# Optimization experiments

Measured on AMD Instinct MI355X. Metric: run time of the kernel, lower is better.

## Reference

```python
import jax, jax.numpy as jnp
import numpy as np


def setup_inputs() -> dict:
    key = jax.random.key(0)
    ks = jax.random.split(key, 6)
    B, S, D = 2, 2048, 1024
    E, DFF = 8, 2048  # E includes always-on expert 0; router sees E-1 routed experts
    scale = 0.02
    return {
        "hidden_states": jax.random.normal(ks[0], (B, S, D), dtype=jnp.float32),
        "router_w": jax.random.normal(ks[1], (D, E - 1), dtype=jnp.float32) * scale,
        "router_b": jnp.zeros((E - 1,), dtype=jnp.float32),
        "wg": jax.random.normal(ks[2], (E, D, DFF), dtype=jnp.float32) * scale,
        "wu": jax.random.normal(ks[3], (E, D, DFF), dtype=jnp.float32) * scale,
        "wd": jax.random.normal(ks[4], (E, DFF, D), dtype=jnp.float32) * scale,
        "top_k": 2,
    }


def _expert_mlp(x, wg_e, wu_e, wd_e):
    # SwiGLU MLP: down( silu(x @ gate) * (x @ up) )
    return (jax.nn.silu(x @ wg_e) * (x @ wu_e)) @ wd_e


def reference(hidden_states, router_w, router_b, wg, wu, wd, top_k):
    B, S, D = hidden_states.shape
    E = wg.shape[0]  # total experts incl. always-on expert 0
    x = hidden_states.reshape(-1, D)  # [T, D]
    T = x.shape[0]

    # Router over E-1 routed experts, softmax in float32
    router_logits = x @ router_w + router_b  # [T, E-1]
    probs = jax.nn.softmax(router_logits.astype(jnp.float32), axis=-1)
    topw, topi = jax.lax.top_k(probs, top_k)  # [T, k]
    topw = topw / jnp.sum(topw, axis=-1, keepdims=True)
    topw = topw.astype(x.dtype)

    # Dense combine weights over routed experts (0 for unselected)
    cw = jnp.zeros((T, E - 1), dtype=x.dtype)
    cw = cw.at[jnp.arange(T)[:, None], topi].add(topw)  # [T, E-1]

    # Always-on expert 0 with weight 1
    out = _expert_mlp(x, wg[0], wu[0], wd[0])  # [T, D]

    # Routed experts 1..E-1 (static small loop over experts)
    for e in range(1, E):
        ye = _expert_mlp(x, wg[e], wu[e], wd[e])  # [T, D]
        out = out + cw[:, e - 1, None] * ye

    return out.reshape(B, S, -1)
```

## Files before the change

kernel.cpp:

```cpp
#include <hip/hip_runtime.h>

#define T_TOK 4096
#define DIM   1024
#define DFF   2048
#define NE    8
#define NR    7
#define MAXNB 71
#define NY    (32 + MAXNB)

typedef __bf16 bf16x8 __attribute__((ext_vector_type(8)));
typedef float  floatx4 __attribute__((ext_vector_type(4)));

__device__ __forceinline__ unsigned short f32_bf16(float f) {
  union { float f; unsigned int u; } v; v.f = f;
  unsigned int u = v.u;
  unsigned int r = (u + 0x7FFFu + ((u >> 16) & 1u)) >> 16;
  return (unsigned short)r;
}

typedef __attribute__((address_space(3))) void lds_void_t;
typedef const __attribute__((address_space(1))) void g_void_t;

__device__ __forceinline__ void gld16(const void* g, void* l) {
  __builtin_amdgcn_global_load_lds((g_void_t*)g, (lds_void_t*)l, 16, 0, 0);
}

__global__ __launch_bounds__(256) void cvt_x_kernel(const float4* __restrict__ in,
                                                    ushort4* __restrict__ out) {
  int i = blockIdx.x * 256 + threadIdx.x;
  float4 v = in[i];
  ushort4 o;
  o.x = f32_bf16(v.x); o.y = f32_bf16(v.y);
  o.z = f32_bf16(v.z); o.w = f32_bf16(v.w);
  out[i] = o;
}

__global__ __launch_bounds__(256) void router_kernel(const float* __restrict__ x,
                                                     const float* __restrict__ rw,
                                                     const float* __restrict__ rb,
                                                     int* __restrict__ idxR,
                                                     float* __restrict__ wslR,
                                                     int* __restrict__ cnt,
                                                     int4* __restrict__ tokE,
                                                     float2* __restrict__ tokW) {
  const int lane = threadIdx.x & 63;
  const int t = blockIdx.x * 4 + (threadIdx.x >> 6);
  const float* xr = x + (size_t)t * DIM;
  float acc[NR];
#pragma unroll
  for (int e = 0; e < NR; e++) acc[e] = 0.f;
  for (int d = lane; d < DIM; d += 64) {
    float xv = xr[d];
#pragma unroll
    for (int e = 0; e < NR; e++) acc[e] += xv * rw[d * NR + e];
  }
#pragma unroll
  for (int off = 32; off > 0; off >>= 1) {
#pragma unroll
    for (int e = 0; e < NR; e++) acc[e] += __shfl_xor(acc[e], off, 64);
  }
  if (lane == 0) {
    float lg[NR];
    float m = -1e30f;
#pragma unroll
    for (int e = 0; e < NR; e++) { lg[e] = acc[e] + rb[e]; m = fmaxf(m, lg[e]); }
    float p[NR], s = 0.f;
#pragma unroll
    for (int e = 0; e < NR; e++) { p[e] = expf(lg[e] - m); s += p[e]; }
#pragma unroll
    for (int e = 0; e < NR; e++) p[e] /= s;
    int i1 = 0;
#pragma unroll
    for (int e = 1; e < NR; e++) if (p[e] > p[i1]) i1 = e;
    int i2 = (i1 == 0) ? 1 : 0;
#pragma unroll
    for (int e = 0; e < NR; e++) if (e != i1 && p[e] > p[i2]) i2 = e;
    float w1 = p[i1], w2 = p[i2], sw = w1 + w2;
    float w1n = w1 / sw, w2n = w2 / sw;
    int s1 = atomicAdd(&cnt[i1], 1);
    idxR[i1 * 4096 + s1] = t; wslR[i1 * 4096 + s1] = w1n;
    int s2 = atomicAdd(&cnt[i2], 1);
    idxR[i2 * 4096 + s2] = t; wslR[i2 * 4096 + s2] = w2n;
    int4 te; te.x = i1; te.y = s1; te.z = i2; te.w = s2;
    tokE[t] = te;
    float2 tw; tw.x = w1n; tw.y = w2n;
    tokW[t] = tw;
  }
}

__global__ __launch_bounds__(256) void sched_kernel(const int* __restrict__ cnt,
                                                    int* __restrict__ idxR,
                                                    float* __restrict__ wslR,
                                                    int4* __restrict__ schedAll,
                                                    int4* __restrict__ schedP,
                                                    int* __restrict__ prefOut,
                                                    int rsb) {
  __shared__ int nb[NR], pref[NR];
  if (threadIdx.x == 0) {
    int p = 0;
    for (int e = 0; e < NR; e++) { int c = cnt[e]; int n = (c + 127) >> 7; nb[e] = n; pref[e] = p; p += n; }
  }
  __syncthreads();
  if (threadIdx.x < NR) prefOut[threadIdx.x] = pref[threadIdx.x];
  for (int e = 0; e < NR; e++) {
    int c = cnt[e], top = nb[e] * 128;
    for (int i = c + (int)threadIdx.x; i < top; i += 256) {
      idxR[e * 4096 + i] = 0; wslR[e * 4096 + i] = 0.f;
    }
  }
  const int NBtot = pref[NR - 1] + nb[NR - 1];
  for (int y = threadIdx.x; y < 32; y += 256) {
    int4 ent; ent.x = 0; ent.y = -1; ent.z = y * 128; ent.w = 0;
    schedAll[y] = ent;
  }
  for (int y = threadIdx.x; y < MAXNB; y += 256) {
    int4 ent; ent.x = -1; ent.y = 0; ent.z = 0; ent.w = 0;
    if (y < NBtot) {
#pragma unroll
      for (int e = 0; e < NR; e++)
        if (y >= pref[e] && y < pref[e] + nb[e]) {
          int rb2 = y - pref[e];
          ent.x = e + 1; ent.y = e * 4096 + rb2 * 128; ent.z = rsb + y * 128;
        }
    }
    schedAll[32 + y] = ent;
  }
  for (int i = threadIdx.x; i < NR * 32; i += 256) {
    int e = i >> 5, rb2 = i & 31;
    int4 ent; ent.w = 0;
    if (rb2 < nb[e]) { ent.x = e + 1; ent.y = e * 4096 + rb2 * 128; ent.z = rb2 * 128; }
    else             { ent.x = -1; ent.y = 0; ent.z = 0; }
    schedP[i] = ent;
  }
}

__global__ __launch_bounds__(256) void transpose_cvt_kernel(
    const float* __restrict__ wg, const float* __restrict__ wu, const float* __restrict__ wd,
    unsigned short* __restrict__ wgt, unsigned short* __restrict__ wut,
    unsigned short* __restrict__ wdt) {
  __shared__ float tile[64][33];
  const int z = blockIdx.z;
  const float* src; unsigned short* dst; int R, C;
  if (z < 8)       { src = wg + (size_t)z * DIM * DFF;        dst = wgt + (size_t)z * DIM * DFF;        R = DIM; C = DFF; }
  else if (z < 16) { src = wu + (size_t)(z - 8) * DIM * DFF;  dst = wut + (size_t)(z - 8) * DIM * DFF;  R = DIM; C = DFF; }
  else             { src = wd + (size_t)(z - 16) * DFF * DIM; dst = wdt + (size_t)(z - 16) * DFF * DIM; R = DFF; C = DIM; }
  const int c0 = blockIdx.x * 32, r0 = blockIdx.y * 64;
  if (c0 >= C || r0 >= R) return;
  const int tx = threadIdx.x & 31, ty = threadIdx.x >> 5;
#pragma unroll
  for (int j = ty; j < 64; j += 8)
    tile[j][tx] = src[(size_t)(r0 + j) * C + c0 + tx];
  __syncthreads();
#pragma unroll
  for (int j = ty; j < 32; j += 8) {
    unsigned int lo = f32_bf16(tile[2 * tx][j]);
    unsigned int hi = f32_bf16(tile[2 * tx + 1][j]);
    *(unsigned int*)(dst + (size_t)(c0 + j) * R + r0 + 2 * tx) = lo | (hi << 16);
  }
}

__global__ __launch_bounds__(512, 2) void gemm1_kernel(
    const unsigned short* __restrict__ xb, const unsigned short* __restrict__ wgt,
    const unsigned short* __restrict__ wut, const int* __restrict__ idxR,
    const int4* __restrict__ sched, unsigned short* __restrict__ h, int gy) {
  const int nblk = gridDim.x;
  int bid = blockIdx.x;
  { int q = nblk >> 3, r = nblk & 7, xc = bid & 7, p = bid >> 3;
    bid = (xc < r ? xc * (q + 1) : r * (q + 1) + (xc - r) * q) + p; }
  const int bx = bid / gy, by = bid - bx * gy;
  const int4 ent = sched[by];
  if (ent.x < 0) return;
  __shared__ unsigned short smem[3 * 24576];
  const int tid = threadIdx.x, lane = tid & 63, wid = tid >> 6;
  const int n0 = bx * 128;
  const int wm64 = (wid >> 2) * 64, wn32 = (wid & 3) * 32;
  const int fr = lane & 15, kq8 = lane >> 4, x7 = fr & 7;
  const int r0 = tid >> 3;
  const int c8 = ((tid & 7) ^ (r0 & 7)) * 8;
  int tok0, tok1;
  if (ent.y < 0) { tok0 = ent.z + r0; tok1 = ent.z + r0 + 64; }
  else           { tok0 = idxR[ent.y + r0]; tok1 = idxR[ent.y + r0 + 64]; }
  const unsigned short* wgt_e = wgt + (size_t)ent.x * DIM * DFF;
  const unsigned short* wut_e = wut + (size_t)ent.x * DIM * DFF;
  const unsigned short* gA0 = xb + (size_t)tok0 * DIM + c8;
  const unsigned short* gA1 = xb + (size_t)tok1 * DIM + c8;
  const unsigned short* gG0 = wgt_e + (size_t)(n0 + r0) * DIM + c8;
  const unsigned short* gG1 = gG0 + (size_t)64 * DIM;
  const unsigned short* gU0 = wut_e + (size_t)(n0 + r0) * DIM + c8;
  const unsigned short* gU1 = gU0 + (size_t)64 * DIM;
  int offA[4][2], offB[2][2];
#pragma unroll
  for (int mi = 0; mi < 4; mi++)
#pragma unroll
    for (int kk = 0; kk < 2; kk++)
      offA[mi][kk] = (wm64 + mi * 16 + fr) * 64 + (((kk * 4 + kq8) ^ x7) * 8);
#pragma unroll
  for (int ni = 0; ni < 2; ni++)
#pragma unroll
    for (int kk = 0; kk < 2; kk++)
      offB[ni][kk] = (wn32 + ni * 16 + fr) * 64 + (((kk * 4 + kq8) ^ x7) * 8);
  floatx4 accg[4][2], accu[4][2];
  const floatx4 z4 = {0.f, 0.f, 0.f, 0.f};
#pragma unroll
  for (int i = 0; i < 4; i++)
#pragma unroll
    for (int j = 0; j < 2; j++) { accg[i][j] = z4; accu[i][j] = z4; }
  {
    unsigned short* d = smem + tid * 8;
    gld16(gA0, d);             gld16(gA1, d + 4096);
    gld16(gG0, d + 8192);      gld16(gG1, d + 12288);
    gld16(gU0, d + 16384);     gld16(gU1, d + 20480);
    unsigned short* e = smem + 24576 + tid * 8;
    gld16(gA0 + 64, e);        gld16(gA1 + 64, e + 4096);
    gld16(gG0 + 64, e + 8192); gld16(gG1 + 64, e + 12288);
    gld16(gU0 + 64, e + 16384); gld16(gU1 + 64, e + 20480);
  }
  asm volatile("s_waitcnt vmcnt(6)" ::: "memory");
  __builtin_amdgcn_s_barrier();
  int b = 0;
  for (int k = 0; k < 16; ++k) {
    const unsigned short* Bb = smem + b * 24576;
    int b2 = b + 2; if (b2 >= 3) b2 -= 3;
    unsigned short* db2 = smem + b2 * 24576 + tid * 8;
    if (k < 14) {
      const int kt = (k + 2) * 64;
      gld16(gA0 + kt, db2);         gld16(gA1 + kt, db2 + 4096);
      gld16(gG0 + kt, db2 + 8192);  gld16(gG1 + kt, db2 + 12288);
      gld16(gU0 + kt, db2 + 16384); gld16(gU1 + kt, db2 + 20480);
    }
    __builtin_amdgcn_sched_barrier(0);
    bf16x8 a[4][2], bg[2][2], bu[2][2];
#pragma unroll
    for (int mi = 0; mi < 4; mi++)
#pragma unroll
      for (int kk = 0; kk < 2; kk++) a[mi][kk] = *(const bf16x8*)(Bb + offA[mi][kk]);
#pragma unroll
    for (int ni = 0; ni < 2; ni++)
#pragma unroll
      for (int kk = 0; kk < 2; kk++) {
        bg[ni][kk] = *(const bf16x8*)(Bb + 8192 + offB[ni][kk]);
        bu[ni][kk] = *(const bf16x8*)(Bb + 16384 + offB[ni][kk]);
      }
    __builtin_amdgcn_s_setprio(1);
#pragma unroll
    for (int mi = 0; mi < 4; mi++)
#pragma unroll
      for (int ni = 0; ni < 2; ni++)
#pragma unroll
        for (int kk = 0; kk < 2; kk++)
          accg[mi][ni] = __builtin_amdgcn_mfma_f32_16x16x32_bf16(a[mi][kk], bg[ni][kk], accg[mi][ni], 0, 0, 0);
#pragma unroll
    for (int mi = 0; mi < 4; mi++)
#pragma unroll
      for (int ni = 0; ni < 2; ni++)
#pragma unroll
        for (int kk = 0; kk < 2; kk++)
          accu[mi][ni] = __builtin_amdgcn_mfma_f32_16x16x32_bf16(a[mi][kk], bu[ni][kk], accu[mi][ni], 0, 0, 0);
    __builtin_amdgcn_s_setprio(0);
    __builtin_amdgcn_sched_barrier(0);
    if (k < 14)       asm volatile("s_waitcnt vmcnt(6)" ::: "memory");
    else if (k == 14) asm volatile("s_waitcnt vmcnt(0)" ::: "memory");
    __builtin_amdgcn_s_barrier();
    b++; if (b == 3) b = 0;
  }
  const int rb = kq8 * 4;
#pragma unroll
  for (int mi = 0; mi < 4; mi++)
#pragma unroll
    for (int ni = 0; ni < 2; ni++)
#pragma unroll
      for (int r = 0; r < 4; r++) {
        int row = ent.z + wm64 + mi * 16 + rb + r;
        int col = n0 + wn32 + ni * 16 + fr;
        float g = accg[mi][ni][r], u = accu[mi][ni][r];
        float hv = (g / (1.f + __expf(-g))) * u;
        h[(size_t)row * DFF + col] = f32_bf16(hv);
      }
}

__global__ __launch_bounds__(512, 2) void gemm2_kernel(
    const unsigned short* __restrict__ hsrc, const unsigned short* __restrict__ wdt,
    const int4* __restrict__ sched, float* __restrict__ y, int gx) {
  const int nblk = gridDim.x;
  int bid = blockIdx.x;
  { int q = nblk >> 3, r = nblk & 7, xc = bid & 7, p = bid >> 3;
    bid = (xc < r ? xc * (q + 1) : r * (q + 1) + (xc - r) * q) + p; }
  const int by = bid / gx, bx = bid - by * gx;
  const int4 ent = sched[by];
  if (ent.x < 0) return;
  __shared__ unsigned short smem[3 * 24576];
  const int tid = threadIdx.x, lane = tid & 63, wid = tid >> 6;
  const int n0 = bx * 256;
  const int wm64 = (wid >> 2) * 64, wn64 = (wid & 3) * 64;
  const int fr = lane & 15, kq8 = lane >> 4, x7 = fr & 7;
  const int r0 = tid >> 3;
  const int c8 = ((tid & 7) ^ (r0 & 7)) * 8;
  const unsigned short* wdt_e = wdt + (size_t)ent.x * DFF * DIM;
  const unsigned short* gA0 = hsrc + (size_t)(ent.z + r0) * DFF + c8;
  const unsigned short* gA1 = gA0 + (size_t)64 * DFF;
  const unsigned short* gB0 = wdt_e + (size_t)(n0 + r0) * DFF + c8;
  const unsigned short* gB1 = gB0 + (size_t)64 * DFF;
  const unsigned short* gB2 = gB0 + (size_t)128 * DFF;
  const unsigned short* gB3 = gB0 + (size_t)192 * DFF;
  int offA[4][2], offB[2][2];
#pragma unroll
  for (int mi = 0; mi < 4; mi++)
#pragma unroll
    for (int kk = 0; kk < 2; kk++)
      offA[mi][kk] = (wm64 + mi * 16 + fr) * 64 + (((kk * 4 + kq8) ^ x7) * 8);
#pragma unroll
  for (int ni = 0; ni < 2; ni++)
#pragma unroll
    for (int kk = 0; kk < 2; kk++)
      offB[ni][kk] = (wn64 + ni * 16 + fr) * 64 + (((kk * 4 + kq8) ^ x7) * 8);
  floatx4 acc[4][4];
  const floatx4 z4 = {0.f, 0.f, 0.f, 0.f};
#pragma unroll
  for (int i = 0; i < 4; i++)
#pragma unroll
    for (int j = 0; j < 4; j++) acc[i][j] = z4;
  {
    unsigned short* d = smem + tid * 8;
    gld16(gA0, d);             gld16(gA1, d + 4096);
    gld16(gB0, d + 8192);      gld16(gB1, d + 12288);
    gld16(gB2, d + 16384);     gld16(gB3, d + 20480);
    unsigned short* e = smem + 24576 + tid * 8;
    gld16(gA0 + 64, e);        gld16(gA1 + 64, e + 4096);
    gld16(gB0 + 64, e + 8192); gld16(gB1 + 64, e + 12288);
    gld16(gB2 + 64, e + 16384); gld16(gB3 + 64, e + 20480);
  }
  asm volatile("s_waitcnt vmcnt(6)" ::: "memory");
  __builtin_amdgcn_s_barrier();
  int b = 0;
  for (int k = 0; k < 32; ++k) {
    const unsigned short* Bb = smem + b * 24576;
    int b2 = b + 2; if (b2 >= 3) b2 -= 3;
    unsigned short* db2 = smem + b2 * 24576 + tid * 8;
    if (k < 30) {
      const int kt = (k + 2) * 64;
      gld16(gA0 + kt, db2);         gld16(gA1 + kt, db2 + 4096);
      gld16(gB0 + kt, db2 + 8192);  gld16(gB1 + kt, db2 + 12288);
      gld16(gB2 + kt, db2 + 16384); gld16(gB3 + kt, db2 + 20480);
    }
    __builtin_amdgcn_sched_barrier(0);
    bf16x8 a[4][2], b0[2][2], b1[2][2];
#pragma unroll
    for (int mi = 0; mi < 4; mi++)
#pragma unroll
      for (int kk = 0; kk < 2; kk++) a[mi][kk] = *(const bf16x8*)(Bb + offA[mi][kk]);
#pragma unroll
    for (int ni = 0; ni < 2; ni++)
#pragma unroll
      for (int kk = 0; kk < 2; kk++) {
        b0[ni][kk] = *(const bf16x8*)(Bb + 8192 + offB[ni][kk]);
        b1[ni][kk] = *(const bf16x8*)(Bb + 10240 + offB[ni][kk]);
      }
    __builtin_amdgcn_s_setprio(1);
#pragma unroll
    for (int mi = 0; mi < 4; mi++)
#pragma unroll
      for (int ni = 0; ni < 2; ni++)
#pragma unroll
        for (int kk = 0; kk < 2; kk++) {
          acc[mi][ni]     = __builtin_amdgcn_mfma_f32_16x16x32_bf16(a[mi][kk], b0[ni][kk], acc[mi][ni], 0, 0, 0);
          acc[mi][2 + ni] = __builtin_amdgcn_mfma_f32_16x16x32_bf16(a[mi][kk], b1[ni][kk], acc[mi][2 + ni], 0, 0, 0);
        }
    __builtin_amdgcn_s_setprio(0);
    __builtin_amdgcn_sched_barrier(0);
    if (k < 30)       asm volatile("s_waitcnt vmcnt(6)" ::: "memory");
    else if (k == 30) asm volatile("s_waitcnt vmcnt(0)" ::: "memory");
    __builtin_amdgcn_s_barrier();
    b++; if (b == 3) b = 0;
  }
  const int rb = kq8 * 4;
#pragma unroll
  for (int mi = 0; mi < 4; mi++)
#pragma unroll
    for (int ni = 0; ni < 4; ni++)
#pragma unroll
      for (int r = 0; r < 4; r++)
        y[(size_t)(ent.z + wm64 + mi * 16 + rb + r) * DIM + n0 + wn64 + ni * 16 + fr] = acc[mi][ni][r];
}

__global__ __launch_bounds__(256) void gemm2_atomic_kernel(
    const unsigned short* __restrict__ h, const unsigned short* __restrict__ wdt,
    const int* __restrict__ idxR, const float* __restrict__ wslR,
    const int4* __restrict__ sched, float* __restrict__ out) {
  const int4 ent = sched[blockIdx.y];
  if (ent.x < 0) return;
  __shared__ unsigned short As[128 * 32];
  __shared__ unsigned short Bs[128 * 32];
  const int tid = threadIdx.x, lane = tid & 63, wid = tid >> 6;
  const int n0 = blockIdx.x * 128;
  const int wm = (wid >> 1) * 64, wn = (wid & 1) * 64;
  floatx4 acc[4][4];
  const floatx4 z4 = {0.f, 0.f, 0.f, 0.f};
#pragma unroll
  for (int i = 0; i < 4; i++)
#pragma unroll
    for (int j = 0; j < 4; j++) acc[i][j] = z4;
  const unsigned short* wdt_e = wdt + (size_t)ent.x * DFF * DIM;
  const int srow = tid >> 2, scol = (tid & 3) * 8;
  const unsigned short* ap0 = h + (size_t)(ent.z + srow) * DFF + scol;
  const unsigned short* ap1 = ap0 + (size_t)64 * DFF;
  const unsigned short* bp0 = wdt_e + (size_t)(n0 + srow) * DFF + scol;
  const unsigned short* bp1 = bp0 + (size_t)64 * DFF;
  unsigned short* as0 = As + tid * 8;
  unsigned short* as1 = As + (256 + tid) * 8;
  unsigned short* bs0 = Bs + tid * 8;
  unsigned short* bs1 = Bs + (256 + tid) * 8;
  const int fr = lane & 15, kq = (lane >> 4) * 8;
  for (int k0 = 0; k0 < DFF; k0 += 32) {
    __syncthreads();
    gld16(ap0 + k0, as0); gld16(ap1 + k0, as1);
    gld16(bp0 + k0, bs0); gld16(bp1 + k0, bs1);
    __syncthreads();
    bf16x8 af[4], bf[4];
#pragma unroll
    for (int mi = 0; mi < 4; mi++) af[mi] = *(const bf16x8*)(As + (wm + mi * 16 + fr) * 32 + kq);
#pragma unroll
    for (int ni = 0; ni < 4; ni++) bf[ni] = *(const bf16x8*)(Bs + (wn + ni * 16 + fr) * 32 + kq);
#pragma unroll
    for (int mi = 0; mi < 4; mi++)
#pragma unroll
      for (int ni = 0; ni < 4; ni++)
        acc[mi][ni] = __builtin_amdgcn_mfma_f32_16x16x32_bf16(af[mi], bf[ni], acc[mi][ni], 0, 0, 0);
  }
  const int rb0 = wm + (lane >> 4) * 4;
  const int cb0 = n0 + wn + fr;
#pragma unroll
  for (int mi = 0; mi < 4; mi++)
#pragma unroll
    for (int r = 0; r < 4; r++) {
      int lrow = rb0 + mi * 16 + r;
      if (ent.y < 0) {
        int tok = ent.z + lrow;
#pragma unroll
        for (int ni = 0; ni < 4; ni++)
          out[(size_t)tok * DIM + cb0 + ni * 16] = acc[mi][ni][r];
      } else {
        int tok = idxR[ent.y + lrow];
        float s = wslR[ent.y + lrow];
        if (s != 0.f) {
#pragma unroll
          for (int ni = 0; ni < 4; ni++)
            atomicAdd(&out[(size_t)tok * DIM + cb0 + ni * 16], s * acc[mi][ni][r]);
        }
      }
    }
}

__global__ __launch_bounds__(256) void combine_kernel(const float* __restrict__ y,
                                                      const int4* __restrict__ tokE,
                                                      const float2* __restrict__ tokW,
                                                      const int* __restrict__ pref,
                                                      float* __restrict__ out) {
  const int t = blockIdx.x;
  const int c = threadIdx.x * 4;
  int4 te = tokE[t];
  float2 tw = tokW[t];
  int p1 = 4096 + pref[te.x] * 128 + te.y;
  int p2 = 4096 + pref[te.z] * 128 + te.w;
  float4 a = *(const float4*)(y + (size_t)t * DIM + c);
  float4 b = *(const float4*)(y + (size_t)p1 * DIM + c);
  float4 d = *(const float4*)(y + (size_t)p2 * DIM + c);
  float4 o;
  o.x = a.x + tw.x * b.x + tw.y * d.x;
  o.y = a.y + tw.x * b.y + tw.y * d.y;
  o.z = a.z + tw.x * b.z + tw.y * d.z;
  o.w = a.w + tw.x * b.w + tw.y * d.w;
  *(float4*)(out + (size_t)t * DIM + c) = o;
}

extern "C" void kernel_launch(void* const* d_in, const int* in_sizes, int n_in,
                              void* d_out, int out_size, void* d_ws, size_t ws_size,
                              hipStream_t stream) {
  const float* x  = (const float*)d_in[0];
  const float* rw = (const float*)d_in[1];
  const float* rb = (const float*)d_in[2];
  const float* wg = (const float*)d_in[3];
  const float* wu = (const float*)d_in[4];
  const float* wd = (const float*)d_in[5];
  float* out = (float*)d_out;

  const bool modeA = ws_size >= (size_t)163300000;
  const bool modeB = !modeA && ws_size >= (size_t)146700000;
  const size_t H_ROWS = modeA ? 13184 : (modeB ? 9088 : 4096);
  const int rsb = modeA ? 4096 : 0;

  char* p = (char*)d_ws;
  unsigned short* xb  = (unsigned short*)p; p += (size_t)T_TOK * DIM * 2;
  unsigned short* h   = (unsigned short*)p; p += H_ROWS * DFF * 2;
  unsigned short* wgt = (unsigned short*)p;
  float*          y   = (float*)p;          p += (size_t)NE * DIM * DFF * 2;
  unsigned short* wut = (unsigned short*)p; p += (size_t)NE * DIM * DFF * 2;
  unsigned short* wdt = (unsigned short*)p; p += (size_t)NE * DIM * DFF * 2;
  int*   idxR = (int*)p;   p += (size_t)NR * 4096 * 4;
  float* wslR;
  if (modeA) { wslR = (float*)wdt; }
  else       { wslR = (float*)p; p += (size_t)NR * 4096 * 4; }
  int*   cnt  = (int*)p;      p += 64;
  int*   pref = (int*)p;      p += 64;
  int4*  schedAll = (int4*)p; p += 2048;
  int4*  schedP   = (int4*)p; p += 4096;
  int4*  tokE = (int4*)p;     p += (size_t)T_TOK * 16;
  float2* tokW = (float2*)p;  p += (size_t)T_TOK * 8;

  cvt_x_kernel<<<dim3(T_TOK * DIM / 4 / 256), 256, 0, stream>>>((const float4*)x, (ushort4*)xb);
  hipMemsetAsync(cnt, 0, 64, stream);
  router_kernel<<<dim3(T_TOK / 4), 256, 0, stream>>>(x, rw, rb, idxR, wslR, cnt, tokE, tokW);
  sched_kernel<<<dim3(1), 256, 0, stream>>>(cnt, idxR, wslR, schedAll, schedP, pref, rsb);
  transpose_cvt_kernel<<<dim3(64, 32, 24), 256, 0, stream>>>(wg, wu, wd, wgt, wut, wdt);

  if (modeA) {
    gemm1_kernel<<<dim3((DFF / 128) * NY), 512, 0, stream>>>(xb, wgt, wut, idxR, schedAll, h, NY);
    gemm2_kernel<<<dim3((DIM / 256) * NY), 512, 0, stream>>>(h, wdt, schedAll, y, DIM / 256);
    combine_kernel<<<dim3(T_TOK), 256, 0, stream>>>(y, tokE, tokW, pref, out);
  } else if (modeB) {
    gemm1_kernel<<<dim3((DFF / 128) * 32), 512, 0, stream>>>(xb, wgt, wut, idxR, schedAll, h, 32);
    gemm2_atomic_kernel<<<dim3(DIM / 128, 32), 256, 0, stream>>>(h, wdt, idxR, wslR, schedAll, out);
    gemm1_kernel<<<dim3((DFF / 128) * MAXNB), 512, 0, stream>>>(xb, wgt, wut, idxR, schedAll + 32, h, MAXNB);
    gemm2_atomic_kernel<<<dim3(DIM / 128, MAXNB), 256, 0, stream>>>(h, wdt, idxR, wslR, schedAll + 32, out);
  } else {
    gemm1_kernel<<<dim3((DFF / 128) * 32), 512, 0, stream>>>(xb, wgt, wut, idxR, schedAll, h, 32);
    gemm2_atomic_kernel<<<dim3(DIM / 128, 32), 256, 0, stream>>>(h, wdt, idxR, wslR, schedAll, out);
    for (int e = 0; e < NR; e++) {
      gemm1_kernel<<<dim3((DFF / 128) * 32), 512, 0, stream>>>(xb, wgt, wut, idxR, schedP + e * 32, h, 32);
      gemm2_atomic_kernel<<<dim3(DIM / 128, 32), 256, 0, stream>>>(h, wdt, idxR, wslR, schedP + e * 32, out);
    }
  }
}
```

Baseline: 546.8 us.

## Widen GEMM N-tiles with K=32 stages and widen weight transpose tiles

The gate/up GEMM now covers 256 output columns per block and the down-projection GEMM covers 512, with each stage shrunk to K=32 and a new swizzled LDS layout. Each wave holds 4x4 (or 4x8) accumulators, so every A fragment feeds more MFMAs and activation re-reads from global memory drop. The weight transpose/convert kernel moves to 64x64 tiles with 8-byte stores. The cost is more registers per wave, twice as many barrier-separated k-steps, and fewer blocks in the grid, which can hurt load balance.

New measurement: 568.5 us. 1.04x slower.

```diff
diff --git a/kernel.cpp b/kernel.cpp
--- a/kernel.cpp
+++ b/kernel.cpp
@@ -7,6 +7,7 @@
 #define NR    7
 #define MAXNB 71
 #define NY    (32 + MAXNB)
+#define G_BUF 20480
 
 typedef __bf16 bf16x8 __attribute__((ext_vector_type(8)));
 typedef float  floatx4 __attribute__((ext_vector_type(4)));
@@ -138,24 +139,26 @@
     const float* __restrict__ wg, const float* __restrict__ wu, const float* __restrict__ wd,
     unsigned short* __restrict__ wgt, unsigned short* __restrict__ wut,
     unsigned short* __restrict__ wdt) {
-  __shared__ float tile[64][33];
+  __shared__ float tile[64][65];
   const int z = blockIdx.z;
   const float* src; unsigned short* dst; int R, C;
   if (z < 8)       { src = wg + (size_t)z * DIM * DFF;        dst = wgt + (size_t)z * DIM * DFF;        R = DIM; C = DFF; }
   else if (z < 16) { src = wu + (size_t)(z - 8) * DIM * DFF;  dst = wut + (size_t)(z - 8) * DIM * DFF;  R = DIM; C = DFF; }
   else             { src = wd + (size_t)(z - 16) * DFF * DIM; dst = wdt + (size_t)(z - 16) * DFF * DIM; R = DFF; C = DIM; }
-  const int c0 = blockIdx.x * 32, r0 = blockIdx.y * 64;
+  const int c0 = blockIdx.x * 64, r0 = blockIdx.y * 64;
   if (c0 >= C || r0 >= R) return;
-  const int tx = threadIdx.x & 31, ty = threadIdx.x >> 5;
-#pragma unroll
-  for (int j = ty; j < 64; j += 8)
+  const int tx = threadIdx.x & 63, ty = threadIdx.x >> 6;
+#pragma unroll
+  for (int j = ty; j < 64; j += 4)
     tile[j][tx] = src[(size_t)(r0 + j) * C + c0 + tx];
   __syncthreads();
-#pragma unroll
-  for (int j = ty; j < 32; j += 8) {
-    unsigned int lo = f32_bf16(tile[2 * tx][j]);
-    unsigned int hi = f32_bf16(tile[2 * tx + 1][j]);
-    *(unsigned int*)(dst + (size_t)(c0 + j) * R + r0 + 2 * tx) = lo | (hi << 16);
+  const int r2 = (threadIdx.x & 15) * 4, jj = threadIdx.x >> 4;
+#pragma unroll
+  for (int j = jj; j < 64; j += 16) {
+    unsigned int lo = (unsigned int)f32_bf16(tile[r2 + 0][j]) | ((unsigned int)f32_bf16(tile[r2 + 1][j]) << 16);
+    unsigned int hi = (unsigned int)f32_bf16(tile[r2 + 2][j]) | ((unsigned int)f32_bf16(tile[r2 + 3][j]) << 16);
+    uint2 o; o.x = lo; o.y = hi;
+    *(uint2*)(dst + (size_t)(c0 + j) * R + r0 + r2) = o;
   }
 }
 
@@ -170,216 +173,188 @@
   const int bx = bid / gy, by = bid - bx * gy;
   const int4 ent = sched[by];
   if (ent.x < 0) return;
-  __shared__ unsigned short smem[3 * 24576];
+  __shared__ unsigned short smem[3 * G_BUF];
   const int tid = threadIdx.x, lane = tid & 63, wid = tid >> 6;
-  const int n0 = bx * 128;
-  const int wm64 = (wid >> 2) * 64, wn32 = (wid & 3) * 32;
-  const int fr = lane & 15, kq8 = lane >> 4, x7 = fr & 7;
-  const int r0 = tid >> 3;
-  const int c8 = ((tid & 7) ^ (r0 & 7)) * 8;
-  int tok0, tok1;
-  if (ent.y < 0) { tok0 = ent.z + r0; tok1 = ent.z + r0 + 64; }
-  else           { tok0 = idxR[ent.y + r0]; tok1 = idxR[ent.y + r0 + 64]; }
+  const int n0 = bx * 256;
+  const int wm = (wid >> 2) * 64;
+  const int wn = (wid & 3) * 64;
+  const int fr = lane & 15, kq = lane >> 4;
+  const int pl = (fr >> 1) * 64 + (((((fr & 1) << 2) | kq) ^ (fr >> 1)) << 3);
+  int offA[4], offG[4], offU[4];
+#pragma unroll
+  for (int mi = 0; mi < 4; mi++) offA[mi] = (wm + mi * 16) * 32 + pl;
+#pragma unroll
+  for (int ni = 0; ni < 4; ni++) {
+    offG[ni] = 4096 + (wn + ni * 16) * 32 + pl;
+    offU[ni] = 12288 + (wn + ni * 16) * 32 + pl;
+  }
+  const int prA = tid >> 3;
+  const int csA = (tid & 7) ^ (prA & 7);
+  const int rowS = 2 * prA + (csA >> 2);
+  const int colS = (csA & 3) * 8;
+  int tokA;
+  if (ent.y < 0) tokA = ent.z + rowS;
+  else           tokA = idxR[ent.y + rowS];
   const unsigned short* wgt_e = wgt + (size_t)ent.x * DIM * DFF;
   const unsigned short* wut_e = wut + (size_t)ent.x * DIM * DFF;
-  const unsigned short* gA0 = xb + (size_t)tok0 * DIM + c8;
-  const unsigned short* gA1 = xb + (size_t)tok1 * DIM + c8;
-  const unsigned short* gG0 = wgt_e + (size_t)(n0 + r0) * DIM + c8;
-  const unsigned short* gG1 = gG0 + (size_t)64 * DIM;
-  const unsigned short* gU0 = wut_e + (size_t)(n0 + r0) * DIM + c8;
-  const unsigned short* gU1 = gU0 + (size_t)64 * DIM;
-  int offA[4][2], offB[2][2];
-#pragma unroll
-  for (int mi = 0; mi < 4; mi++)
-#pragma unroll
-    for (int kk = 0; kk < 2; kk++)
-      offA[mi][kk] = (wm64 + mi * 16 + fr) * 64 + (((kk * 4 + kq8) ^ x7) * 8);
-#pragma unroll
-  for (int ni = 0; ni < 2; ni++)
-#pragma unroll
-    for (int kk = 0; kk < 2; kk++)
-      offB[ni][kk] = (wn32 + ni * 16 + fr) * 64 + (((kk * 4 + kq8) ^ x7) * 8);
-  floatx4 accg[4][2], accu[4][2];
+  const unsigned short* gA  = xb + (size_t)tokA * DIM + colS;
+  const unsigned short* gG0 = wgt_e + (size_t)(n0 + rowS) * DIM + colS;
+  const unsigned short* gG1 = gG0 + (size_t)128 * DIM;
+  const unsigned short* gU0 = wut_e + (size_t)(n0 + rowS) * DIM + colS;
+  const unsigned short* gU1 = gU0 + (size_t)128 * DIM;
+  floatx4 accg[4][4], accu[4][4];
   const floatx4 z4 = {0.f, 0.f, 0.f, 0.f};
 #pragma unroll
   for (int i = 0; i < 4; i++)
 #pragma unroll
-    for (int j = 0; j < 2; j++) { accg[i][j] = z4; accu[i][j] = z4; }
+    for (int j = 0; j < 4; j++) { accg[i][j] = z4; accu[i][j] = z4; }
   {
     unsigned short* d = smem + tid * 8;
-    gld16(gA0, d);             gld16(gA1, d + 4096);
-    gld16(gG0, d + 8192);      gld16(gG1, d + 12288);
-    gld16(gU0, d + 16384);     gld16(gU1, d + 20480);
-    unsigned short* e = smem + 24576 + tid * 8;
-    gld16(gA0 + 64, e);        gld16(gA1 + 64, e + 4096);
-    gld16(gG0 + 64, e + 8192); gld16(gG1 + 64, e + 12288);
-    gld16(gU0 + 64, e + 16384); gld16(gU1 + 64, e + 20480);
-  }
-  asm volatile("s_waitcnt vmcnt(6)" ::: "memory");
+    gld16(gA, d); gld16(gG0, d + 4096); gld16(gG1, d + 8192);
+    gld16(gU0, d + 12288); gld16(gU1, d + 16384);
+    unsigned short* e = smem + G_BUF + tid * 8;
+    gld16(gA + 32, e); gld16(gG0 + 32, e + 4096); gld16(gG1 + 32, e + 8192);
+    gld16(gU0 + 32, e + 12288); gld16(gU1 + 32, e + 16384);
+  }
+  asm volatile("s_waitcnt vmcnt(5)" ::: "memory");
   __builtin_amdgcn_s_barrier();
   int b = 0;
-  for (int k = 0; k < 16; ++k) {
-    const unsigned short* Bb = smem + b * 24576;
+  for (int k = 0; k < 32; ++k) {
+    const unsigned short* Bb = smem + b * G_BUF;
     int b2 = b + 2; if (b2 >= 3) b2 -= 3;
-    unsigned short* db2 = smem + b2 * 24576 + tid * 8;
-    if (k < 14) {
-      const int kt = (k + 2) * 64;
-      gld16(gA0 + kt, db2);         gld16(gA1 + kt, db2 + 4096);
-      gld16(gG0 + kt, db2 + 8192);  gld16(gG1 + kt, db2 + 12288);
-      gld16(gU0 + kt, db2 + 16384); gld16(gU1 + kt, db2 + 20480);
+    unsigned short* db2 = smem + b2 * G_BUF + tid * 8;
+    if (k < 30) {
+      const int kt = (k + 2) * 32;
+      gld16(gA + kt, db2); gld16(gG0 + kt, db2 + 4096); gld16(gG1 + kt, db2 + 8192);
+      gld16(gU0 + kt, db2 + 12288); gld16(gU1 + kt, db2 + 16384);
     }
     __builtin_amdgcn_sched_barrier(0);
-    bf16x8 a[4][2], bg[2][2], bu[2][2];
+    bf16x8 a[4], g[4], u[4];
+#pragma unroll
+    for (int mi = 0; mi < 4; mi++) a[mi] = *(const bf16x8*)(Bb + offA[mi]);
+#pragma unroll
+    for (int ni = 0; ni < 4; ni++) {
+      g[ni] = *(const bf16x8*)(Bb + offG[ni]);
+      u[ni] = *(const bf16x8*)(Bb + offU[ni]);
+    }
+    __builtin_amdgcn_s_setprio(1);
 #pragma unroll
     for (int mi = 0; mi < 4; mi++)
 #pragma unroll
-      for (int kk = 0; kk < 2; kk++) a[mi][kk] = *(const bf16x8*)(Bb + offA[mi][kk]);
-#pragma unroll
-    for (int ni = 0; ni < 2; ni++)
-#pragma unroll
-      for (int kk = 0; kk < 2; kk++) {
-        bg[ni][kk] = *(const bf16x8*)(Bb + 8192 + offB[ni][kk]);
-        bu[ni][kk] = *(const bf16x8*)(Bb + 16384 + offB[ni][kk]);
-      }
-    __builtin_amdgcn_s_setprio(1);
+      for (int ni = 0; ni < 4; ni++)
+        accg[mi][ni] = __builtin_amdgcn_mfma_f32_16x16x32_bf16(a[mi], g[ni], accg[mi][ni], 0, 0, 0);
 #pragma unroll
     for (int mi = 0; mi < 4; mi++)
 #pragma unroll
-      for (int ni = 0; ni < 2; ni++)
-#pragma unroll
-        for (int kk = 0; kk < 2; kk++)
-          accg[mi][ni] = __builtin_amdgcn_mfma_f32_16x16x32_bf16(a[mi][kk], bg[ni][kk], accg[mi][ni], 0, 0, 0);
-#pragma unroll
-    for (int mi = 0; mi < 4; mi++)
-#pragma unroll
-      for (int ni = 0; ni < 2; ni++)
-#pragma unroll
-        for (int kk = 0; kk < 2; kk++)
-          accu[mi][ni] = __builtin_amdgcn_mfma_f32_16x16x32_bf16(a[mi][kk], bu[ni][kk], accu[mi][ni], 0, 0, 0);
+      for (int ni = 0; ni < 4; ni++)
+        accu[mi][ni] = __builtin_amdgcn_mfma_f32_16x16x32_bf16(a[mi], u[ni], accu[mi][ni], 0, 0, 0);
     __builtin_amdgcn_s_setprio(0);
     __builtin_amdgcn_sched_barrier(0);
-    if (k < 14)       asm volatile("s_waitcnt vmcnt(6)" ::: "memory");
-    else if (k == 14) asm volatile("s_waitcnt vmcnt(0)" ::: "memory");
+    if (k < 30)       asm volatile("s_waitcnt vmcnt(5)" ::: "memory");
+    else if (k == 30) asm volatile("s_waitcnt vmcnt(0)" ::: "memory");
     __builtin_amdgcn_s_barrier();
     b++; if (b == 3) b = 0;
   }
-  const int rb = kq8 * 4;
+  const int rb = kq * 4;
 #pragma unroll
   for (int mi = 0; mi < 4; mi++)
 #pragma unroll
-    for (int ni = 0; ni < 2; ni++)
+    for (int ni = 0; ni < 4; ni++)
 #pragma unroll
       for (int r = 0; r < 4; r++) {
-        int row = ent.z + wm64 + mi * 16 + rb + r;
-        int col = n0 + wn32 + ni * 16 + fr;
-        float g = accg[mi][ni][r], u = accu[mi][ni][r];
-        float hv = (g / (1.f + __expf(-g))) * u;
+        int row = ent.z + wm + mi * 16 + rb + r;
+        int col = n0 + wn + ni * 16 + fr;
+        float gv = accg[mi][ni][r], uv = accu[mi][ni][r];
+        float hv = (gv / (1.f + __expf(-gv))) * uv;
         h[(size_t)row * DFF + col] = f32_bf16(hv);
       }
 }
 
 __global__ __launch_bounds__(512, 2) void gemm2_kernel(
     const unsigned short* __restrict__ hsrc, const unsigned short* __restrict__ wdt,
-    const int4* __restrict__ sched, float* __restrict__ y, int gx) {
+    const int4* __restrict__ sched, float* __restrict__ y, int gy) {
   const int nblk = gridDim.x;
   int bid = blockIdx.x;
   { int q = nblk >> 3, r = nblk & 7, xc = bid & 7, p = bid >> 3;
     bid = (xc < r ? xc * (q + 1) : r * (q + 1) + (xc - r) * q) + p; }
-  const int by = bid / gx, bx = bid - by * gx;
+  const int bx = bid / gy, by = bid - bx * gy;
   const int4 ent = sched[by];
   if (ent.x < 0) return;
-  __shared__ unsigned short smem[3 * 24576];
+  __shared__ unsigned short smem[3 * G_BUF];
   const int tid = threadIdx.x, lane = tid & 63, wid = tid >> 6;
-  const int n0 = bx * 256;
-  const int wm64 = (wid >> 2) * 64, wn64 = (wid & 3) * 64;
-  const int fr = lane & 15, kq8 = lane >> 4, x7 = fr & 7;
-  const int r0 = tid >> 3;
-  const int c8 = ((tid & 7) ^ (r0 & 7)) * 8;
+  const int n0 = bx * 512;
+  const int wm = (wid >> 2) * 64;
+  const int wn = (wid & 3) * 128;
+  const int fr = lane & 15, kq = lane >> 4;
+  const int pl = (fr >> 1) * 64 + (((((fr & 1) << 2) | kq) ^ (fr >> 1)) << 3);
+  int offA[4], offB[8];
+#pragma unroll
+  for (int mi = 0; mi < 4; mi++) offA[mi] = (wm + mi * 16) * 32 + pl;
+#pragma unroll
+  for (int ni = 0; ni < 8; ni++) offB[ni] = 4096 + (wn + ni * 16) * 32 + pl;
+  const int prA = tid >> 3;
+  const int csA = (tid & 7) ^ (prA & 7);
+  const int rowS = 2 * prA + (csA >> 2);
+  const int colS = (csA & 3) * 8;
   const unsigned short* wdt_e = wdt + (size_t)ent.x * DFF * DIM;
-  const unsigned short* gA0 = hsrc + (size_t)(ent.z + r0) * DFF + c8;
-  const unsigned short* gA1 = gA0 + (size_t)64 * DFF;
-  const unsigned short* gB0 = wdt_e + (size_t)(n0 + r0) * DFF + c8;
-  const unsigned short* gB1 = gB0 + (size_t)64 * DFF;
-  const unsigned short* gB2 = gB0 + (size_t)128 * DFF;
-  const unsigned short* gB3 = gB0 + (size_t)192 * DFF;
-  int offA[4][2], offB[2][2];
-#pragma unroll
-  for (int mi = 0; mi < 4; mi++)
-#pragma unroll
-    for (int kk = 0; kk < 2; kk++)
-      offA[mi][kk] = (wm64 + mi * 16 + fr) * 64 + (((kk * 4 + kq8) ^ x7) * 8);
-#pragma unroll
-  for (int ni = 0; ni < 2; ni++)
-#pragma unroll
-    for (int kk = 0; kk < 2; kk++)
-      offB[ni][kk] = (wn64 + ni * 16 + fr) * 64 + (((kk * 4 + kq8) ^ x7) * 8);
-  floatx4 acc[4][4];
+  const unsigned short* gA  = hsrc + (size_t)(ent.z + rowS) * DFF + colS;
+  const unsigned short* gB0 = wdt_e + (size_t)(n0 + rowS) * DFF + colS;
+  const unsigned short* gB1 = gB0 + (size_t)128 * DFF;
+  const unsigned short* gB2 = gB0 + (size_t)256 * DFF;
+  const unsigned short* gB3 = gB0 + (size_t)384 * DFF;
+  floatx4 acc[4][8];
   const floatx4 z4 = {0.f, 0.f, 0.f, 0.f};
 #pragma unroll
   for (int i = 0; i < 4; i++)
 #pragma unroll
-    for (int j = 0; j < 4; j++) acc[i][j] = z4;
+    for (int j = 0; j < 8; j++) acc[i][j] = z4;
   {
     unsigned short* d = smem + tid * 8;
-    gld16(gA0, d);             gld16(gA1, d + 4096);
-    gld16(gB0, d + 8192);      gld16(gB1, d + 12288);
-    gld16(gB2, d + 16384);     gld16(gB3, d + 20480);
-    unsigned short* e = smem + 24576 + tid * 8;
-    gld16(gA0 + 64, e);        gld16(gA1 + 64, e + 4096);
-    gld16(gB0 + 64, e + 8192); gld16(gB1 + 64, e + 12288);
-    gld16(gB2 + 64, e + 16384); gld16(gB3 + 64, e + 20480);
-  }
-  asm volatile("s_waitcnt vmcnt(6)" ::: "memory");
+    gld16(gA, d); gld16(gB0, d + 4096); gld16(gB1, d + 8192);
+    gld16(gB2, d + 12288); gld16(gB3, d + 16384);
+    unsigned short* e = smem + G_BUF + tid * 8;
+    gld16(gA + 32, e); gld16(gB0 + 32, e + 4096); gld16(gB1 + 32, e + 8192);
+    gld16(gB2 + 32, e + 12288); gld16(gB3 + 32, e + 16384);
+  }
+  asm volatile("s_waitcnt vmcnt(5)" ::: "memory");
   __builtin_amdgcn_s_barrier();
   int b = 0;
-  for (int k = 0; k < 32; ++k) {
-    const unsigned short* Bb = smem + b * 24576;
+  for (int k = 0; k < 64; ++k) {
+    const unsigned short* Bb = smem + b * G_BUF;
     int b2 = b + 2; if (b2 >= 3) b2 -= 3;
-    unsigned short* db2 = smem + b2 * 24576 + tid * 8;
-    if (k < 30) {
-      const int kt = (k + 2) * 64;
-      gld16(gA0 + kt, db2);         gld16(gA1 + kt, db2 + 4096);
-      gld16(gB0 + kt, db2 + 8192);  gld16(gB1 + kt, db2 + 12288);
-      gld16(gB2 + kt, db2 + 16384); gld16(gB3 + kt, db2 + 20480);
+    unsigned short* db2 = smem + b2 * G_BUF + tid * 8;
+    if (k < 62) {
+      const int kt = (k + 2) * 32;
+      gld16(gA + kt, db2); gld16(gB0 + kt, db2 + 4096); gld16(gB1 + kt, db2 + 8192);
+      gld16(gB2 + kt, db2 + 12288); gld16(gB3 + kt, db2 + 16384);
     }
     __builtin_amdgcn_sched_barrier(0);
-    bf16x8 a[4][2], b0[2][2], b1[2][2];
+    bf16x8 a[4], bf[8];
+#pragma unroll
+    for (int mi = 0; mi < 4; mi++) a[mi] = *(const bf16x8*)(Bb + offA[mi]);
+#pragma unroll
+    for (int ni = 0; ni < 8; ni++) bf[ni] = *(const bf16x8*)(Bb + offB[ni]);
+    __builtin_amdgcn_s_setprio(1);
 #pragma unroll
     for (int mi = 0; mi < 4; mi++)
 #pragma unroll
-      for (int kk = 0; kk < 2; kk++) a[mi][kk] = *(const bf16x8*)(Bb + offA[mi][kk]);
-#pragma unroll
-    for (int ni = 0; ni < 2; ni++)
-#pragma unroll
-      for (int kk = 0; kk < 2; kk++) {
-        b0[ni][kk] = *(const bf16x8*)(Bb + 8192 + offB[ni][kk]);
-        b1[ni][kk] = *(const bf16x8*)(Bb + 10240 + offB[ni][kk]);
-      }
-    __builtin_amdgcn_s_setprio(1);
-#pragma unroll
-    for (int mi = 0; mi < 4; mi++)
-#pragma unroll
-      for (int ni = 0; ni < 2; ni++)
-#pragma unroll
-        for (int kk = 0; kk < 2; kk++) {
-          acc[mi][ni]     = __builtin_amdgcn_mfma_f32_16x16x32_bf16(a[mi][kk], b0[ni][kk], acc[mi][ni], 0, 0, 0);
-          acc[mi][2 + ni] = __builtin_amdgcn_mfma_f32_16x16x32_bf16(a[mi][kk], b1[ni][kk], acc[mi][2 + ni], 0, 0, 0);
-        }
+      for (int ni = 0; ni < 8; ni++)
+        acc[mi][ni] = __builtin_amdgcn_mfma_f32_16x16x32_bf16(a[mi], bf[ni], acc[mi][ni], 0, 0, 0);
     __builtin_amdgcn_s_setprio(0);
     __builtin_amdgcn_sched_barrier(0);
-    if (k < 30)       asm volatile("s_waitcnt vmcnt(6)" ::: "memory");
-    else if (k == 30) asm volatile("s_waitcnt vmcnt(0)" ::: "memory");
+    if (k < 62)       asm volatile("s_waitcnt vmcnt(5)" ::: "memory");
+    else if (k == 62) asm volatile("s_waitcnt vmcnt(0)" ::: "memory");
     __builtin_amdgcn_s_barrier();
     b++; if (b == 3) b = 0;
   }
-  const int rb = kq8 * 4;
+  const int rb = kq * 4;
 #pragma unroll
   for (int mi = 0; mi < 4; mi++)
 #pragma unroll
-    for (int ni = 0; ni < 4; ni++)
+    for (int ni = 0; ni < 8; ni++)
 #pragma unroll
       for (int r = 0; r < 4; r++)
-        y[(size_t)(ent.z + wm64 + mi * 16 + rb + r) * DIM + n0 + wn64 + ni * 16 + fr] = acc[mi][ni][r];
+        y[(size_t)(ent.z + wm + mi * 16 + rb + r) * DIM + n0 + wn + ni * 16 + fr] = acc[mi][ni][r];
 }
 
 __global__ __launch_bounds__(256) void gemm2_atomic_kernel(
@@ -510,22 +485,22 @@
   hipMemsetAsync(cnt, 0, 64, stream);
   router_kernel<<<dim3(T_TOK / 4), 256, 0, stream>>>(x, rw, rb, idxR, wslR, cnt, tokE, tokW);
   sched_kernel<<<dim3(1), 256, 0, stream>>>(cnt, idxR, wslR, schedAll, schedP, pref, rsb);
-  transpose_cvt_kernel<<<dim3(64, 32, 24), 256, 0, stream>>>(wg, wu, wd, wgt, wut, wdt);
+  transpose_cvt_kernel<<<dim3(32, 32, 24), 256, 0, stream>>>(wg, wu, wd, wgt, wut, wdt);
 
   if (modeA) {
-    gemm1_kernel<<<dim3((DFF / 128) * NY), 512, 0, stream>>>(xb, wgt, wut, idxR, schedAll, h, NY);
-    gemm2_kernel<<<dim3((DIM / 256) * NY), 512, 0, stream>>>(h, wdt, schedAll, y, DIM / 256);
+    gemm1_kernel<<<dim3((DFF / 256) * NY), 512, 0, stream>>>(xb, wgt, wut, idxR, schedAll, h, NY);
+    gemm2_kernel<<<dim3((DIM / 512) * NY), 512, 0, stream>>>(h, wdt, schedAll, y, NY);
     combine_kernel<<<dim3(T_TOK), 256, 0, stream>>>(y, tokE, tokW, pref, out);
   } else if (modeB) {
-    gemm1_kernel<<<dim3((DFF / 128) * 32), 512, 0, stream>>>(xb, wgt, wut, idxR, schedAll, h, 32);
+    gemm1_kernel<<<dim3((DFF / 256) * 32), 512, 0, stream>>>(xb, wgt, wut, idxR, schedAll, h, 32);
     gemm2_atomic_kernel<<<dim3(DIM / 128, 32), 256, 0, stream>>>(h, wdt, idxR, wslR, schedAll, out);
-    gemm1_kernel<<<dim3((DFF / 128) * MAXNB), 512, 0, stream>>>(xb, wgt, wut, idxR, schedAll + 32, h, MAXNB);
+    gemm1_kernel<<<dim3((DFF / 256) * MAXNB), 512, 0, stream>>>(xb, wgt, wut, idxR, schedAll + 32, h, MAXNB);
     gemm2_atomic_kernel<<<dim3(DIM / 128, MAXNB), 256, 0, stream>>>(h, wdt, idxR, wslR, schedAll + 32, out);
   } else {
-    gemm1_kernel<<<dim3((DFF / 128) * 32), 512, 0, stream>>>(xb, wgt, wut, idxR, schedAll, h, 32);
+    gemm1_kernel<<<dim3((DFF / 256) * 32), 512, 0, stream>>>(xb, wgt, wut, idxR, schedAll, h, 32);
     gemm2_atomic_kernel<<<dim3(DIM / 128, 32), 256, 0, stream>>>(h, wdt, idxR, wslR, schedAll, out);
     for (int e = 0; e < NR; e++) {
-      gemm1_kernel<<<dim3((DFF / 128) * 32), 512, 0, stream>>>(xb, wgt, wut, idxR, schedP + e * 32, h, 32);
+      gemm1_kernel<<<dim3((DFF / 256) * 32), 512, 0, stream>>>(xb, wgt, wut, idxR, schedP + e * 32, h, 32);
       gemm2_atomic_kernel<<<dim3(DIM / 128, 32), 256, 0, stream>>>(h, wdt, idxR, wslR, schedP + e * 32, out);
     }
   }
```
